# Performance work log

Hardware: AMD Instinct MI355X
Metric: run time of the kernel (lower is better)

The kernel has to match this reference:

```python
import jax, jax.numpy as jnp
import numpy as np

N_EMBD = 2048
N_HEAD = 16
HEAD_DIM = N_EMBD // N_HEAD
BATCH = 2
SEQ = 2048


def setup_inputs() -> dict:
    key = jax.random.key(0)
    k1, k2, k3 = jax.random.split(key, 3)
    scale = 0.02
    return {
        "hidden_states": jax.random.normal(k1, (BATCH, SEQ, N_EMBD), dtype=jnp.float32),
        "c_attn_w": jax.random.normal(k2, (N_EMBD, 3 * N_EMBD), dtype=jnp.float32) * scale,
        "c_attn_b": jnp.zeros((3 * N_EMBD,), dtype=jnp.float32),
        "c_proj_w": jax.random.normal(k3, (N_EMBD, N_EMBD), dtype=jnp.float32) * scale,
        "c_proj_b": jnp.zeros((N_EMBD,), dtype=jnp.float32),
    }


def reference(hidden_states, c_attn_w, c_attn_b, c_proj_w, c_proj_b):
    B, S, E = hidden_states.shape
    # Fused QKV projection (Conv1D: x @ W + b)
    qkv = hidden_states @ c_attn_w + c_attn_b  # [B, S, 3E]
    q, k, v = jnp.split(qkv, 3, axis=-1)
    # split heads -> [B, H, S, D]
    def split_heads(t):
        return t.reshape(B, S, N_HEAD, HEAD_DIM).transpose(0, 2, 1, 3)
    q, k, v = split_heads(q), split_heads(k), split_heads(v)
    # scaled scores, causal mask, softmax (dropout p=0 -> identity)
    scores = jnp.einsum("bhqd,bhkd->bhqk", q, k) / jnp.asarray(
        HEAD_DIM ** 0.5, dtype=q.dtype)
    causal = jnp.tril(jnp.ones((S, S), dtype=bool))  # [S, S]
    mask_value = jnp.finfo(scores.dtype).min
    scores = jnp.where(causal[None, None, :, :], scores, mask_value)
    attn = jax.nn.softmax(scores, axis=-1)
    out = jnp.einsum("bhqk,bhkd->bhqd", attn, v)  # [B, H, S, D]
    # merge heads -> [B, S, E]
    out = out.transpose(0, 2, 1, 3).reshape(B, S, E)
    # output projection
    return out @ c_proj_w + c_proj_b
```

## Files before the change

### kernel.cpp

```cpp
#include <hip/hip_runtime.h>
#include <hip/hip_bf16.h>

typedef __bf16 bf16x8 __attribute__((ext_vector_type(8)));
typedef float f32x4 __attribute__((ext_vector_type(4)));

__device__ __forceinline__ float bf2f(unsigned short u) {
  union { unsigned int i; float f; } v; v.i = ((unsigned int)u) << 16; return v.f;
}
__device__ __forceinline__ unsigned short f2bf(float f) {
  union { unsigned int i; float f; } v; v.f = f;
  unsigned int i = v.i;
  return (unsigned short)((i + 0x7FFFu + ((i >> 16) & 1u)) >> 16);
}

typedef const __attribute__((address_space(1))) unsigned int* gas_ptr;
typedef __attribute__((address_space(3))) unsigned int* las_ptr;
__device__ __forceinline__ void gload_lds16(const unsigned short* g, unsigned short* l) {
  __builtin_amdgcn_global_load_lds((gas_ptr)(const void*)g, (las_ptr)(void*)l, 16, 0, 0);
}

__global__ __launch_bounds__(256) void detect_k(const unsigned short* __restrict__ h,
                                                int* __restrict__ flag) {
  __shared__ int s[256];
  int cnt = 0;
  for (int i = threadIdx.x; i < 4096; i += 256) {
    unsigned short u = h[2 * i];
    int e = (u >> 7) & 0xFF;
    if ((e >= 96 && e <= 140) || u == 0) cnt++;
  }
  s[threadIdx.x] = cnt;
  __syncthreads();
  for (int o = 128; o > 0; o >>= 1) {
    if (threadIdx.x < o) s[threadIdx.x] += s[threadIdx.x + o];
    __syncthreads();
  }
  if (threadIdx.x == 0) *flag = (s[0] >= 3600) ? 1 : 0;
}

__global__ __launch_bounds__(256) void cvt_k(const void* __restrict__ src,
                                             unsigned short* __restrict__ dst, int n,
                                             const int* __restrict__ flag) {
  const int f = *flag;
  for (int i = blockIdx.x * 256 + threadIdx.x; i < n; i += gridDim.x * 256)
    dst[i] = f ? ((const unsigned short*)src)[i] : f2bf(((const float*)src)[i]);
}

__global__ __launch_bounds__(256) void transpose_cvt_k(const void* __restrict__ src,
                                                       unsigned short* __restrict__ dst,
                                                       int R, int C,
                                                       const int* __restrict__ flag) {
  __shared__ unsigned short tile[32][33];
  const int f = *flag;
  const int x = threadIdx.x & 31;
  const int y = threadIdx.x >> 5;
  const int r0 = blockIdx.y * 32, c0 = blockIdx.x * 32;
#pragma unroll
  for (int i = 0; i < 4; i++) {
    size_t idx = (size_t)(r0 + y + 8 * i) * C + c0 + x;
    tile[y + 8 * i][x] = f ? ((const unsigned short*)src)[idx]
                           : f2bf(((const float*)src)[idx]);
  }
  __syncthreads();
#pragma unroll
  for (int i = 0; i < 4; i++)
    dst[(size_t)(c0 + y + 8 * i) * R + r0 + x] = tile[x][y + 8 * i];
}

__global__ __launch_bounds__(256) void transpose_v_k(const unsigned short* __restrict__ qkv,
                                                     unsigned short* __restrict__ Vt) {
  __shared__ unsigned short tile[32][33];
  const int bh = blockIdx.z;
  const int b = bh >> 4, hh = bh & 15;
  const int s0 = blockIdx.x * 32, d0 = blockIdx.y * 32;
  const int x = threadIdx.x & 31, y = threadIdx.x >> 5;
#pragma unroll
  for (int i = 0; i < 4; i++)
    tile[y + 8 * i][x] =
        qkv[((size_t)b * 2048 + s0 + y + 8 * i) * 6144 + 4096 + hh * 128 + d0 + x];
  __syncthreads();
#pragma unroll
  for (int i = 0; i < 4; i++)
    Vt[((size_t)bh * 128 + d0 + y + 8 * i) * 2048 + s0 + x] = tile[x][y + 8 * i];
}

__global__ __launch_bounds__(256) void gemm_bias_k(const unsigned short* __restrict__ A,
                                                   const unsigned short* __restrict__ Bt,
                                                   const unsigned short* __restrict__ bias,
                                                   void* __restrict__ Cout,
                                                   int M, int N, int K,
                                                   const int* __restrict__ flag,
                                                   int final_out) {
  __shared__ __attribute__((aligned(16))) unsigned short As[128][64];
  __shared__ __attribute__((aligned(16))) unsigned short Bs[128][64];
  const int t = threadIdx.x;
  const int wave = t >> 6, lane = t & 63;
  const int col = lane & 15, quad = lane >> 4;
  const int wm = wave >> 1, wn = wave & 1;
  const int m0 = blockIdx.y * 128, n0 = blockIdx.x * 128;
  const int srow = lane >> 3;
  const int schunk = ((lane & 7) ^ srow) * 8;
  const int rsw = col & 7;

  const f32x4 fzero = {0.f, 0.f, 0.f, 0.f};
  f32x4 acc[4][4];
#pragma unroll
  for (int i = 0; i < 4; i++)
#pragma unroll
    for (int j = 0; j < 4; j++) acc[i][j] = fzero;

  for (int k0 = 0; k0 < K; k0 += 64) {
    __syncthreads();
#pragma unroll
    for (int c = 0; c < 4; c++) {
      int seg = wave * 4 + c;
      int row = seg * 8 + srow;
      gload_lds16(&A [(size_t)(m0 + row) * K + k0 + schunk], &As[seg * 8][0]);
      gload_lds16(&Bt[(size_t)(n0 + row) * K + k0 + schunk], &Bs[seg * 8][0]);
    }
    __syncthreads();
#pragma unroll
    for (int ks = 0; ks < 2; ks++) {
      bf16x8 af[4], bfr[4];
#pragma unroll
      for (int i = 0; i < 4; i++)
        af[i] = *(const bf16x8*)&As[wm * 64 + i * 16 + col][(((ks << 2) | quad) ^ rsw) * 8];
#pragma unroll
      for (int j = 0; j < 4; j++)
        bfr[j] = *(const bf16x8*)&Bs[wn * 64 + j * 16 + col][(((ks << 2) | quad) ^ rsw) * 8];
#pragma unroll
      for (int i = 0; i < 4; i++)
#pragma unroll
        for (int j = 0; j < 4; j++)
          acc[i][j] = __builtin_amdgcn_mfma_f32_16x16x32_bf16(af[i], bfr[j], acc[i][j], 0, 0, 0);
    }
  }
  const int f32o = final_out ? (*flag == 0) : 0;
#pragma unroll
  for (int j = 0; j < 4; j++) {
    int n = n0 + wn * 64 + j * 16 + col;
    float bv = bf2f(bias[n]);
#pragma unroll
    for (int i = 0; i < 4; i++)
#pragma unroll
      for (int r = 0; r < 4; r++) {
        int m = m0 + wm * 64 + i * 16 + quad * 4 + r;
        float v = acc[i][j][r] + bv;
        if (f32o) ((float*)Cout)[(size_t)m * N + n] = v;
        else      ((unsigned short*)Cout)[(size_t)m * N + n] = f2bf(v);
      }
  }
}

#define ATT_SCALE 0.08838834764831845f
__global__ __launch_bounds__(256) void attn_k(const unsigned short* __restrict__ qkv,
                                              const unsigned short* __restrict__ Vt,
                                              unsigned short* __restrict__ O) {
  __shared__ __attribute__((aligned(16))) unsigned short Ks[64][136];
  __shared__ __attribute__((aligned(16))) unsigned short Vs[128][72];
  __shared__ __attribute__((aligned(16))) unsigned short Ps[4][16][72];
  const int t = threadIdx.x;
  const int wave = t >> 6, lane = t & 63;
  const int col = lane & 15, quad = lane >> 4;
  const int h = blockIdx.y, b = blockIdx.z;
  const size_t base = (size_t)b * 2048 * 6144;
  const size_t vbase = ((size_t)(b * 16 + h)) * 128 * 2048;
  const int hcol = h * 128;

  const int kr = t >> 2;
  const int kc = (t & 3) * 8;
  const int vr = t >> 1;
  const int vc = (t & 1) * 32;

  const f32x4 fzero = {0.f, 0.f, 0.f, 0.f};

  for (int pass = 0; pass < 2; pass++) {
    const int qt = pass ? (int)blockIdx.x : 31 - (int)blockIdx.x;

    bf16x8 qf[4];
    {
      size_t qrow = base + (size_t)(qt * 64 + wave * 16 + col) * 6144 + hcol;
#pragma unroll
      for (int ks = 0; ks < 4; ks++)
        qf[ks] = *(const bf16x8*)&qkv[qrow + ks * 32 + quad * 8];
    }

    f32x4 o[8];
#pragma unroll
    for (int i = 0; i < 8; i++) o[i] = fzero;
    float l_i[4] = {0.f, 0.f, 0.f, 0.f};

    __syncthreads();
    {
      size_t grow = base + (size_t)kr * 6144 + 2048 + hcol;
#pragma unroll
      for (int p = 0; p < 4; p++)
        *(bf16x8*)&Ks[kr][kc + p * 32] = *(const bf16x8*)&qkv[grow + kc + p * 32];
      size_t vrow = vbase + (size_t)vr * 2048;
#pragma unroll
      for (int c = 0; c < 4; c++)
        *(bf16x8*)&Vs[vr][vc + c * 8] = *(const bf16x8*)&Vt[vrow + vc + c * 8];
    }
    __syncthreads();

    for (int kt = 0; kt <= qt; kt++) {
      bf16x8 kreg[4], vreg[4];
      const bool pf = (kt < qt);
      if (pf) {
        size_t grow = base + (size_t)((kt + 1) * 64 + kr) * 6144 + 2048 + hcol;
#pragma unroll
        for (int p = 0; p < 4; p++)
          kreg[p] = *(const bf16x8*)&qkv[grow + kc + p * 32];
        size_t vrow = vbase + (size_t)vr * 2048 + (kt + 1) * 64;
#pragma unroll
        for (int c = 0; c < 4; c++)
          vreg[c] = *(const bf16x8*)&Vt[vrow + vc + c * 8];
      }

      f32x4 sc[4];
#pragma unroll
      for (int nb = 0; nb < 4; nb++) {
        f32x4 s = fzero;
#pragma unroll
        for (int ks = 0; ks < 4; ks++) {
          bf16x8 kf = *(const bf16x8*)&Ks[nb * 16 + col][ks * 32 + quad * 8];
          s = __builtin_amdgcn_mfma_f32_16x16x32_bf16(qf[ks], kf, s, 0, 0, 0);
        }
        sc[nb] = s;
      }

      const bool diag = (kt == qt);
#pragma unroll
      for (int nb = 0; nb < 4; nb++) {
        int kl = nb * 16 + col;
#pragma unroll
        for (int r = 0; r < 4; r++) {
          float s = sc[nb][r];
          if (diag && kl > wave * 16 + quad * 4 + r) s = -1e30f;
          float p = __expf(s * ATT_SCALE);
          l_i[r] += p;
          Ps[wave][quad * 4 + r][nb * 16 + col] = f2bf(p);
        }
      }
      bf16x8 pfr[2];
#pragma unroll
      for (int ks2 = 0; ks2 < 2; ks2++)
        pfr[ks2] = *(const bf16x8*)&Ps[wave][col][ks2 * 32 + quad * 8];
#pragma unroll
      for (int nbo = 0; nbo < 8; nbo++)
#pragma unroll
        for (int ks2 = 0; ks2 < 2; ks2++) {
          bf16x8 vf = *(const bf16x8*)&Vs[nbo * 16 + col][ks2 * 32 + quad * 8];
          o[nbo] = __builtin_amdgcn_mfma_f32_16x16x32_bf16(pfr[ks2], vf, o[nbo], 0, 0, 0);
        }

      __syncthreads();
      if (pf) {
#pragma unroll
        for (int p = 0; p < 4; p++)
          *(bf16x8*)&Ks[kr][kc + p * 32] = kreg[p];
#pragma unroll
        for (int c = 0; c < 4; c++)
          *(bf16x8*)&Vs[vr][vc + c * 8] = vreg[c];
      }
      __syncthreads();
    }

#pragma unroll
    for (int r = 0; r < 4; r++) {
#pragma unroll
      for (int off = 1; off < 16; off <<= 1)
        l_i[r] += __shfl_xor(l_i[r], off, 64);
      l_i[r] = 1.0f / l_i[r];
    }

#pragma unroll
    for (int nbo = 0; nbo < 8; nbo++)
#pragma unroll
      for (int r = 0; r < 4; r++) {
        int m = qt * 64 + wave * 16 + quad * 4 + r;
        O[((size_t)b * 2048 + m) * 2048 + hcol + nbo * 16 + col] = f2bf(o[nbo][r] * l_i[r]);
      }
  }
}

extern "C" void kernel_launch(void* const* d_in, const int* in_sizes, int n_in,
                              void* d_out, int out_size, void* d_ws, size_t ws_size,
                              hipStream_t stream) {
  (void)in_sizes; (void)n_in; (void)out_size; (void)ws_size;
  int* flag = (int*)d_ws;
  unsigned short* wsu = (unsigned short*)d_ws + 128;
  unsigned short* Wt_qkv    = wsu;
  unsigned short* Wt_proj   = Wt_qkv + (size_t)6144 * 2048;
  unsigned short* QKV       = Wt_proj + (size_t)2048 * 2048;
  unsigned short* hidden_bf = QKV + (size_t)4096 * 6144;
  unsigned short* bias_q    = hidden_bf + (size_t)4096 * 2048;
  unsigned short* bias_p    = bias_q + 6144;
  unsigned short* Obuf      = Wt_qkv;
  unsigned short* Vt        = hidden_bf;

  detect_k<<<1, 256, 0, stream>>>((const unsigned short*)d_in[0], flag);
  cvt_k<<<4096, 256, 0, stream>>>(d_in[0], hidden_bf, 4096 * 2048, flag);
  cvt_k<<<24, 256, 0, stream>>>(d_in[2], bias_q, 6144, flag);
  cvt_k<<<8, 256, 0, stream>>>(d_in[4], bias_p, 2048, flag);
  transpose_cvt_k<<<dim3(192, 64), 256, 0, stream>>>(d_in[1], Wt_qkv, 2048, 6144, flag);
  transpose_cvt_k<<<dim3(64, 64), 256, 0, stream>>>(d_in[3], Wt_proj, 2048, 2048, flag);
  gemm_bias_k<<<dim3(48, 32), 256, 0, stream>>>(hidden_bf, Wt_qkv, bias_q, QKV,
                                                4096, 6144, 2048, flag, 0);
  transpose_v_k<<<dim3(64, 4, 32), 256, 0, stream>>>(QKV, Vt);
  attn_k<<<dim3(16, 16, 2), 256, 0, stream>>>(QKV, Vt, Obuf);
  gemm_bias_k<<<dim3(16, 32), 256, 0, stream>>>(Obuf, Wt_proj, bias_p, d_out,
                                                4096, 2048, 2048, flag, 1);
}
```

Measured before the change: 427.3 us.

## Switch attention to 32x32x16 MFMA with 128-row query tiles and chunked LDS layout

The attention kernel now gives each block 128 query rows (32 per wave) instead of 64, using 32x32x16 bf16 MFMA for both QK^T and PV. K, V and P tiles are stored in LDS in a k-chunked [chunk][row][8] layout so fragment reads are contiguous, and waves whose rows lie entirely before a key tile skip its compute. The grid is halved to 8x16x2, keeping two-pass load balancing. Larger tiles halve K/V reloads per query row, but accumulators grow to 64 floats plus 16 row sums per lane, raising register pressure, and there are fewer blocks to fill the GPU.

```diff
diff --git a/kernel.cpp b/kernel.cpp
--- a/kernel.cpp
+++ b/kernel.cpp
@@ -3,6 +3,7 @@
 
 typedef __bf16 bf16x8 __attribute__((ext_vector_type(8)));
 typedef float f32x4 __attribute__((ext_vector_type(4)));
+typedef float f32x16 __attribute__((ext_vector_type(16)));
 
 __device__ __forceinline__ float bf2f(unsigned short u) {
   union { unsigned int i; float f; } v; v.i = ((unsigned int)u) << 16; return v.f;
@@ -155,12 +156,12 @@
 __global__ __launch_bounds__(256) void attn_k(const unsigned short* __restrict__ qkv,
                                               const unsigned short* __restrict__ Vt,
                                               unsigned short* __restrict__ O) {
-  __shared__ __attribute__((aligned(16))) unsigned short Ks[64][136];
-  __shared__ __attribute__((aligned(16))) unsigned short Vs[128][72];
-  __shared__ __attribute__((aligned(16))) unsigned short Ps[4][16][72];
+  __shared__ __attribute__((aligned(16))) unsigned short Ks2[16][64][8];
+  __shared__ __attribute__((aligned(16))) unsigned short Vs2[8][128][8];
+  __shared__ __attribute__((aligned(16))) unsigned short Ps2[4][8][32][8];
   const int t = threadIdx.x;
   const int wave = t >> 6, lane = t & 63;
-  const int col = lane & 15, quad = lane >> 4;
+  const int l31 = lane & 31, hw = lane >> 5;
   const int h = blockIdx.y, b = blockIdx.z;
   const size_t base = (size_t)b * 2048 * 6144;
   const size_t vbase = ((size_t)(b * 16 + h)) * 128 * 2048;
@@ -171,40 +172,44 @@
   const int vr = t >> 1;
   const int vc = (t & 1) * 32;
 
-  const f32x4 fzero = {0.f, 0.f, 0.f, 0.f};
-
   for (int pass = 0; pass < 2; pass++) {
-    const int qt = pass ? (int)blockIdx.x : 31 - (int)blockIdx.x;
-
-    bf16x8 qf[4];
+    const int qt = pass ? (int)blockIdx.x : 15 - (int)blockIdx.x;
+    const int nkt = 2 * qt + 2;
+    const int qrow0 = qt * 128 + wave * 32;
+
+    bf16x8 qf[8];
     {
-      size_t qrow = base + (size_t)(qt * 64 + wave * 16 + col) * 6144 + hcol;
-#pragma unroll
-      for (int ks = 0; ks < 4; ks++)
-        qf[ks] = *(const bf16x8*)&qkv[qrow + ks * 32 + quad * 8];
-    }
-
-    f32x4 o[8];
-#pragma unroll
-    for (int i = 0; i < 8; i++) o[i] = fzero;
-    float l_i[4] = {0.f, 0.f, 0.f, 0.f};
+      size_t qrow = base + (size_t)(qrow0 + l31) * 6144 + hcol;
+#pragma unroll
+      for (int ks = 0; ks < 8; ks++)
+        qf[ks] = *(const bf16x8*)&qkv[qrow + ks * 16 + hw * 8];
+    }
+
+    f32x16 o[4];
+#pragma unroll
+    for (int i = 0; i < 4; i++)
+#pragma unroll
+      for (int r = 0; r < 16; r++) o[i][r] = 0.f;
+    float l_acc[16];
+#pragma unroll
+    for (int r = 0; r < 16; r++) l_acc[r] = 0.f;
 
     __syncthreads();
     {
       size_t grow = base + (size_t)kr * 6144 + 2048 + hcol;
 #pragma unroll
       for (int p = 0; p < 4; p++)
-        *(bf16x8*)&Ks[kr][kc + p * 32] = *(const bf16x8*)&qkv[grow + kc + p * 32];
+        *(bf16x8*)&Ks2[(kc >> 3) + p * 4][kr][0] = *(const bf16x8*)&qkv[grow + kc + p * 32];
       size_t vrow = vbase + (size_t)vr * 2048;
 #pragma unroll
       for (int c = 0; c < 4; c++)
-        *(bf16x8*)&Vs[vr][vc + c * 8] = *(const bf16x8*)&Vt[vrow + vc + c * 8];
-    }
-    __syncthreads();
-
-    for (int kt = 0; kt <= qt; kt++) {
+        *(bf16x8*)&Vs2[(vc >> 3) + c][vr][0] = *(const bf16x8*)&Vt[vrow + vc + c * 8];
+    }
+    __syncthreads();
+
+    for (int kt = 0; kt < nkt; kt++) {
       bf16x8 kreg[4], vreg[4];
-      const bool pf = (kt < qt);
+      const bool pf = (kt + 1 < nkt);
       if (pf) {
         size_t grow = base + (size_t)((kt + 1) * 64 + kr) * 6144 + 2048 + hcol;
 #pragma unroll
@@ -216,69 +221,70 @@
           vreg[c] = *(const bf16x8*)&Vt[vrow + vc + c * 8];
       }
 
-      f32x4 sc[4];
-#pragma unroll
-      for (int nb = 0; nb < 4; nb++) {
-        f32x4 s = fzero;
-#pragma unroll
-        for (int ks = 0; ks < 4; ks++) {
-          bf16x8 kf = *(const bf16x8*)&Ks[nb * 16 + col][ks * 32 + quad * 8];
-          s = __builtin_amdgcn_mfma_f32_16x16x32_bf16(qf[ks], kf, s, 0, 0, 0);
+      const bool active = (kt * 64 < qrow0 + 32);
+      if (active) {
+        f32x16 sc[2];
+#pragma unroll
+        for (int nb = 0; nb < 2; nb++)
+#pragma unroll
+          for (int r = 0; r < 16; r++) sc[nb][r] = 0.f;
+#pragma unroll
+        for (int ks = 0; ks < 8; ks++)
+#pragma unroll
+          for (int nb = 0; nb < 2; nb++) {
+            bf16x8 kf = *(const bf16x8*)&Ks2[ks * 2 + hw][nb * 32 + l31][0];
+            sc[nb] = __builtin_amdgcn_mfma_f32_32x32x16_bf16(qf[ks], kf, sc[nb], 0, 0, 0);
+          }
+
+#pragma unroll
+        for (int nb = 0; nb < 2; nb++) {
+          const int key = kt * 64 + nb * 32 + l31;
+#pragma unroll
+          for (int r = 0; r < 16; r++) {
+            const int row = (r & 3) + 8 * (r >> 2) + 4 * hw;
+            float p = (key <= qrow0 + row) ? __expf(sc[nb][r] * ATT_SCALE) : 0.f;
+            l_acc[r] += p;
+            Ps2[wave][nb * 4 + (l31 >> 3)][row][l31 & 7] = f2bf(p);
+          }
         }
-        sc[nb] = s;
-      }
-
-      const bool diag = (kt == qt);
-#pragma unroll
-      for (int nb = 0; nb < 4; nb++) {
-        int kl = nb * 16 + col;
-#pragma unroll
-        for (int r = 0; r < 4; r++) {
-          float s = sc[nb][r];
-          if (diag && kl > wave * 16 + quad * 4 + r) s = -1e30f;
-          float p = __expf(s * ATT_SCALE);
-          l_i[r] += p;
-          Ps[wave][quad * 4 + r][nb * 16 + col] = f2bf(p);
+#pragma unroll
+        for (int ks2 = 0; ks2 < 4; ks2++) {
+          bf16x8 pa = *(const bf16x8*)&Ps2[wave][ks2 * 2 + hw][l31][0];
+#pragma unroll
+          for (int nbo = 0; nbo < 4; nbo++) {
+            bf16x8 vf = *(const bf16x8*)&Vs2[ks2 * 2 + hw][nbo * 32 + l31][0];
+            o[nbo] = __builtin_amdgcn_mfma_f32_32x32x16_bf16(pa, vf, o[nbo], 0, 0, 0);
+          }
         }
       }
-      bf16x8 pfr[2];
-#pragma unroll
-      for (int ks2 = 0; ks2 < 2; ks2++)
-        pfr[ks2] = *(const bf16x8*)&Ps[wave][col][ks2 * 32 + quad * 8];
-#pragma unroll
-      for (int nbo = 0; nbo < 8; nbo++)
-#pragma unroll
-        for (int ks2 = 0; ks2 < 2; ks2++) {
-          bf16x8 vf = *(const bf16x8*)&Vs[nbo * 16 + col][ks2 * 32 + quad * 8];
-          o[nbo] = __builtin_amdgcn_mfma_f32_16x16x32_bf16(pfr[ks2], vf, o[nbo], 0, 0, 0);
-        }
 
       __syncthreads();
       if (pf) {
 #pragma unroll
         for (int p = 0; p < 4; p++)
-          *(bf16x8*)&Ks[kr][kc + p * 32] = kreg[p];
+          *(bf16x8*)&Ks2[(kc >> 3) + p * 4][kr][0] = kreg[p];
 #pragma unroll
         for (int c = 0; c < 4; c++)
-          *(bf16x8*)&Vs[vr][vc + c * 8] = vreg[c];
+          *(bf16x8*)&Vs2[(vc >> 3) + c][vr][0] = vreg[c];
       }
       __syncthreads();
     }
 
 #pragma unroll
-    for (int r = 0; r < 4; r++) {
-#pragma unroll
-      for (int off = 1; off < 16; off <<= 1)
-        l_i[r] += __shfl_xor(l_i[r], off, 64);
-      l_i[r] = 1.0f / l_i[r];
-    }
-
-#pragma unroll
-    for (int nbo = 0; nbo < 8; nbo++)
-#pragma unroll
-      for (int r = 0; r < 4; r++) {
-        int m = qt * 64 + wave * 16 + quad * 4 + r;
-        O[((size_t)b * 2048 + m) * 2048 + hcol + nbo * 16 + col] = f2bf(o[nbo][r] * l_i[r]);
+    for (int r = 0; r < 16; r++) {
+#pragma unroll
+      for (int off = 1; off < 32; off <<= 1)
+        l_acc[r] += __shfl_xor(l_acc[r], off, 64);
+      l_acc[r] = 1.0f / l_acc[r];
+    }
+
+#pragma unroll
+    for (int nbo = 0; nbo < 4; nbo++)
+#pragma unroll
+      for (int r = 0; r < 16; r++) {
+        const int row = (r & 3) + 8 * (r >> 2) + 4 * hw;
+        O[((size_t)b * 2048 + qrow0 + row) * 2048 + hcol + nbo * 32 + l31] =
+            f2bf(o[nbo][r] * l_acc[r]);
       }
   }
 }
@@ -307,7 +313,7 @@
   gemm_bias_k<<<dim3(48, 32), 256, 0, stream>>>(hidden_bf, Wt_qkv, bias_q, QKV,
                                                 4096, 6144, 2048, flag, 0);
   transpose_v_k<<<dim3(64, 4, 32), 256, 0, stream>>>(QKV, Vt);
-  attn_k<<<dim3(16, 16, 2), 256, 0, stream>>>(QKV, Vt, Obuf);
+  attn_k<<<dim3(8, 16, 2), 256, 0, stream>>>(QKV, Vt, Obuf);
   gemm_bias_k<<<dim3(16, 32), 256, 0, stream>>>(Obuf, Wt_proj, bias_p, d_out,
                                                 4096, 2048, 2048, flag, 1);
 }
```

New measurement: 446.9 us. 1.05x slower.
